# Kernel tuning notes

Measured on AMD Instinct MI355X. Metric: run time of the kernel, lower is better.

Reference implementation:

```python
import jax, jax.numpy as jnp
import numpy as np

N, NUM_ST, NUM_LT = 8, 256, 4096
C_ST, C_LT, C_LAT = 512, 512, 128
LN_EPS = 1e-3  # keras LayerNormalization default epsilon


def setup_inputs() -> dict:
    key = jax.random.key(0)
    ks = jax.random.split(key, 12)
    w = lambda k, shape, sc=0.05: jax.random.normal(k, shape, jnp.float32) * sc
    return {
        "st_feat": jax.random.normal(ks[0], (N, NUM_ST, 1, 1, C_ST), jnp.float32),
        "lt_feat": jax.random.normal(ks[1], (N, NUM_LT, 1, 1, C_LT), jnp.float32),
        # conv1x1 kernels stored as (in, out) matrices
        "w_st": w(ks[2], (C_ST, C_LAT)),
        "b_st": w(ks[3], (C_LAT,), 0.01),
        "w_lt": w(ks[4], (C_LT, C_LAT)),
        "b_lt": w(ks[5], (C_LAT,), 0.01),
        "w_g": w(ks[6], (C_LT, C_LAT)),
        "b_g": w(ks[7], (C_LAT,), 0.01),
        # LayerNorm over axes [1,2,3,4] of (n, C_LAT, NUM_ST, 1, 1)
        "ln_gamma": 1.0 + w(ks[8], (C_LAT, NUM_ST, 1, 1), 0.02),
        "ln_beta": w(ks[9], (C_LAT, NUM_ST, 1, 1), 0.02),
        # out_conv: Conv3D on tensor with last dim 1 -> in_channels=1, kernel (out,)
        "w_out": w(ks[10], (C_ST,)),
        "b_out": w(ks[11], (C_ST,), 0.01),
    }


def reference(st_feat, lt_feat, w_st, b_st, w_lt, b_lt, w_g, b_g,
              ln_gamma, ln_beta, w_out, b_out):
    n = st_feat.shape[0]
    # 1x1x1 conv projections == matmul over last (channel) dim
    theta = jnp.einsum('nshwc,cd->nshwd', st_feat, w_st) + b_st  # (n,S,1,1,c)
    phi = jnp.einsum('nlhwc,cd->nlhwd', lt_feat, w_lt) + b_lt    # (n,L,1,1,c)
    g = jnp.einsum('nlhwc,cd->nlhwd', lt_feat, w_g) + b_g        # (n,L,1,1,c)
    # Faithful raw reshapes (row-major reinterpretation, as in the TF code)
    theta = theta.reshape(n, C_LAT, NUM_ST)
    phi = phi.reshape(n, C_LAT, NUM_LT)
    g = g.reshape(n, C_LAT, NUM_LT)
    # theta^T @ phi  -> (n, S, L)
    attn = jnp.einsum('ncs,ncl->nsl', theta, phi)
    attn = attn / jnp.sqrt(jnp.asarray(C_LAT, jnp.float32))  # use_scale
    p = jax.nn.softmax(attn, axis=-1)
    # g @ p^T -> (n, c, S)
    out = jnp.einsum('ncl,nsl->ncs', g, p)
    out = out.reshape(n, C_LAT, NUM_ST, 1, 1)
    # pre_activate: LayerNorm over all non-batch axes, then ReLU
    mean = jnp.mean(out, axis=(1, 2, 3, 4), keepdims=True)
    var = jnp.var(out, axis=(1, 2, 3, 4), keepdims=True)
    out = (out - mean) * jax.lax.rsqrt(var + LN_EPS) * ln_gamma + ln_beta
    out = jax.nn.relu(out)
    # out_conv: last dim is 1 -> broadcasts to C_ST output channels
    out = out * w_out + b_out  # (n, C_LAT, NUM_ST, 1, C_ST)
    # dropout is identity at inference
    return out
```

## Files before the change

kernel.cpp:

```cpp
#include <hip/hip_runtime.h>
#include <cstdint>

typedef unsigned short u16;
typedef unsigned int u32;
typedef __attribute__((ext_vector_type(8))) __bf16 bf16x8;
typedef __attribute__((ext_vector_type(4))) float f32x4;

__device__ __forceinline__ u32 f2bf_bits(float x) {
    u32 a = __builtin_bit_cast(u32, x);
    a += 0x7FFFu + ((a >> 16) & 1u);
    return a >> 16;
}
__device__ __forceinline__ u32 pack2(float lo, float hi) {
    u32 a = __builtin_bit_cast(u32, lo);
    u32 b = __builtin_bit_cast(u32, hi);
    a += 0x7FFFu + ((a >> 16) & 1u);
    b += 0x7FFFu + ((b >> 16) & 1u);
    return (a >> 16) | (b & 0xFFFF0000u);
}

#define LDS_STRIDE 72

__global__ __launch_bounds__(256) void k_prep(
    const float* __restrict__ w_lt, const float* __restrict__ w_g,
    u16* __restrict__ wltT, u16* __restrict__ wgT,
    const float* __restrict__ st, const float* __restrict__ w_st,
    const float* __restrict__ b_st, u16* __restrict__ thT,
    float* __restrict__ stats)
{
    __shared__ float sA[8 * 512];
    int bi = blockIdx.x;
    int tid = threadIdx.x;
    if (bi < 512) {
        int idx = bi * 256 + tid;
        int which = idx >> 16;
        int rem = idx & 65535;
        int nrow = rem >> 9;
        int k = rem & 511;
        const float* src = which ? w_g : w_lt;
        u16* dst = which ? wgT : wltT;
        dst[rem] = (u16)f2bf_bits(src[k * 128 + nrow]);
        return;
    }
    if (bi == 768) {
        if (tid < 16) stats[tid] = 0.f;
        return;
    }
    int r0 = (bi - 512) * 8;
    {
        const float4* src = (const float4*)(st + (size_t)r0 * 512);
        float4* dst = (float4*)sA;
        #pragma unroll
        for (int i = 0; i < 4; i++) dst[tid + i * 256] = src[tid + i * 256];
    }
    __syncthreads();
    int d = tid & 127, rh = tid >> 7;
    float acc[4] = {0.f, 0.f, 0.f, 0.f};
    #pragma unroll 4
    for (int k = 0; k < 512; k++) {
        float w = w_st[(size_t)k * 128 + d];
        #pragma unroll
        for (int j = 0; j < 4; j++) acc[j] += sA[(rh + j * 2) * 512 + k] * w;
    }
    float bias = b_st[d];
    #pragma unroll
    for (int j = 0; j < 4; j++) {
        int r = r0 + rh + j * 2;
        int n_idx = r >> 8, s_raw = r & 255;
        int f = s_raw * 128 + d;
        thT[(size_t)n_idx * 32768 + (size_t)(f & 255) * 128 + (f >> 8)] =
            (u16)f2bf_bits(acc[j] + bias);
    }
}

__global__ __launch_bounds__(256, 2) void k1_proj_lt(
    const float* __restrict__ lt,
    const u16* __restrict__ wltT, const u16* __restrict__ wgT,
    const float* __restrict__ b_lt, const float* __restrict__ b_g,
    u16* __restrict__ phi, u16* __restrict__ g)
{
    __shared__ u16 sA[128 * LDS_STRIDE];
    __shared__ u16 sBl[128 * LDS_STRIDE];
    __shared__ u16 sBg[128 * LDS_STRIDE];
    int tid = threadIdx.x;
    int wave = tid >> 6, lane = tid & 63, quad = lane >> 4, lq = lane & 15;
    int m0 = blockIdx.x * 128;
    int srow = tid >> 1, skc = (tid & 1) * 32;

    f32x4 zero = {0.f, 0.f, 0.f, 0.f};
    f32x4 acc[2][2][8];
    for (int p = 0; p < 2; p++)
        for (int mt = 0; mt < 2; mt++)
            for (int nt = 0; nt < 8; nt++) acc[p][mt][nt] = zero;

    for (int ko = 0; ko < 8; ko++) {
        {
            const float4* src = (const float4*)(lt + (size_t)(m0 + srow) * 512 + ko * 64 + skc);
            uint2* dst = (uint2*)&sA[srow * LDS_STRIDE + skc];
            #pragma unroll
            for (int i = 0; i < 8; i++) {
                float4 v = src[i];
                uint2 u; u.x = pack2(v.x, v.y); u.y = pack2(v.z, v.w);
                dst[i] = u;
            }
        }
        {
            const uint4* srcl = (const uint4*)(wltT + srow * 512 + ko * 64 + skc);
            const uint4* srcg = (const uint4*)(wgT  + srow * 512 + ko * 64 + skc);
            uint4* dstl = (uint4*)&sBl[srow * LDS_STRIDE + skc];
            uint4* dstg = (uint4*)&sBg[srow * LDS_STRIDE + skc];
            #pragma unroll
            for (int i = 0; i < 4; i++) { dstl[i] = srcl[i]; dstg[i] = srcg[i]; }
        }
        __syncthreads();
        #pragma unroll
        for (int kk = 0; kk < 2; kk++) {
            bf16x8 a[2], bl[8], bg[8];
            #pragma unroll
            for (int mt = 0; mt < 2; mt++)
                a[mt] = *(const bf16x8*)&sA[(wave * 32 + mt * 16 + lq) * LDS_STRIDE + kk * 32 + quad * 8];
            #pragma unroll
            for (int nt = 0; nt < 8; nt++) {
                bl[nt] = *(const bf16x8*)&sBl[(nt * 16 + lq) * LDS_STRIDE + kk * 32 + quad * 8];
                bg[nt] = *(const bf16x8*)&sBg[(nt * 16 + lq) * LDS_STRIDE + kk * 32 + quad * 8];
            }
            #pragma unroll
            for (int mt = 0; mt < 2; mt++)
                #pragma unroll
                for (int nt = 0; nt < 8; nt++) {
                    acc[0][mt][nt] = __builtin_amdgcn_mfma_f32_16x16x32_bf16(a[mt], bl[nt], acc[0][mt][nt], 0, 0, 0);
                    acc[1][mt][nt] = __builtin_amdgcn_mfma_f32_16x16x32_bf16(a[mt], bg[nt], acc[1][mt][nt], 0, 0, 0);
                }
        }
        __syncthreads();
    }
    #pragma unroll
    for (int mt = 0; mt < 2; mt++) {
        int mbase = m0 + wave * 32 + mt * 16 + quad * 4;
        #pragma unroll
        for (int nt = 0; nt < 8; nt++) {
            int n = nt * 16 + lq;
            float biasl = b_lt[n], biasg = b_g[n];
            #pragma unroll
            for (int r = 0; r < 4; r++) {
                size_t o = (size_t)(mbase + r) * 128 + n;
                phi[o] = (u16)f2bf_bits(acc[0][mt][nt][r] + biasl);
                g[o]   = (u16)f2bf_bits(acc[1][mt][nt][r] + biasg);
            }
        }
    }
}

__global__ __launch_bounds__(256) void k_tr(const u16* __restrict__ phi, u16* __restrict__ phiT)
{
    __shared__ u16 s[64 * 65];
    int bi = blockIdx.x;
    int n_idx = bi >> 7, rem = bi & 127;
    int c0 = (rem >> 6) * 64, l0 = (rem & 63) * 64;
    const u16* src = phi + (size_t)n_idx * 524288;
    u16* dst = phiT + (size_t)n_idx * 524288;
    int t = threadIdx.x;
    #pragma unroll
    for (int i = 0; i < 2; i++) {
        int idx = t + i * 256;
        int row = idx >> 3;
        int col = (idx & 7) * 8;
        uint4 v = *(const uint4*)(src + (size_t)(c0 + row) * 4096 + l0 + col);
        u16 tmp[8];
        *(uint4*)tmp = v;
        #pragma unroll
        for (int j = 0; j < 8; j++) s[row * 65 + col + j] = tmp[j];
    }
    __syncthreads();
    #pragma unroll
    for (int i = 0; i < 2; i++) {
        int idx = t + i * 256;
        int lrow = idx >> 3;
        int cb = (idx & 7) * 8;
        u16 tmp[8];
        #pragma unroll
        for (int j = 0; j < 8; j++) tmp[j] = s[(cb + j) * 65 + lrow];
        *(uint4*)(dst + (size_t)(l0 + lrow) * 128 + c0 + cb) = *(uint4*)tmp;
    }
}

__global__ __launch_bounds__(256, 2) void k3_attn(
    const u16* __restrict__ thT, const u16* __restrict__ phiT,
    float* __restrict__ attn)
{
    __shared__ u16 sA[128 * LDS_STRIDE];
    __shared__ u16 sB[128 * LDS_STRIDE];
    int tid = threadIdx.x;
    int wave = tid >> 6, lane = tid & 63, quad = lane >> 4, lq = lane & 15;
    int bi = blockIdx.x;
    int n_idx = bi >> 6, rem = bi & 63;
    int m0 = (rem >> 5) * 128;
    int l0 = (rem & 31) * 128;
    const u16* Ab = thT + (size_t)n_idx * 32768;
    const u16* Bb = phiT + (size_t)n_idx * 524288;
    int srow = tid >> 1, skc = (tid & 1) * 32;

    f32x4 zero = {0.f, 0.f, 0.f, 0.f};
    f32x4 acc[2][8];
    for (int mt = 0; mt < 2; mt++)
        for (int nt = 0; nt < 8; nt++) acc[mt][nt] = zero;

    for (int ko = 0; ko < 2; ko++) {
        const uint4* srcA = (const uint4*)(Ab + (size_t)(m0 + srow) * 128 + ko * 64 + skc);
        const uint4* srcB = (const uint4*)(Bb + (size_t)(l0 + srow) * 128 + ko * 64 + skc);
        uint4* dA = (uint4*)&sA[srow * LDS_STRIDE + skc];
        uint4* dB = (uint4*)&sB[srow * LDS_STRIDE + skc];
        #pragma unroll
        for (int i = 0; i < 4; i++) { dA[i] = srcA[i]; dB[i] = srcB[i]; }
        __syncthreads();
        #pragma unroll
        for (int kk = 0; kk < 2; kk++) {
            bf16x8 a[2], b[8];
            #pragma unroll
            for (int mt = 0; mt < 2; mt++)
                a[mt] = *(const bf16x8*)&sA[(wave * 32 + mt * 16 + lq) * LDS_STRIDE + kk * 32 + quad * 8];
            #pragma unroll
            for (int nt = 0; nt < 8; nt++)
                b[nt] = *(const bf16x8*)&sB[(nt * 16 + lq) * LDS_STRIDE + kk * 32 + quad * 8];
            #pragma unroll
            for (int mt = 0; mt < 2; mt++)
                #pragma unroll
                for (int nt = 0; nt < 8; nt++)
                    acc[mt][nt] = __builtin_amdgcn_mfma_f32_16x16x32_bf16(a[mt], b[nt], acc[mt][nt], 0, 0, 0);
        }
        __syncthreads();
    }
    const float scale = 0.08838834764831845f;
    float* Cb = attn + (size_t)n_idx * 1048576;
    #pragma unroll
    for (int mt = 0; mt < 2; mt++) {
        int mbase = m0 + wave * 32 + mt * 16 + quad * 4;
        #pragma unroll
        for (int nt = 0; nt < 8; nt++) {
            int col = l0 + nt * 16 + lq;
            #pragma unroll
            for (int r = 0; r < 4; r++)
                Cb[(size_t)(mbase + r) * 4096 + col] = acc[mt][nt][r] * scale;
        }
    }
}

__global__ __launch_bounds__(256) void k4_stats(
    const float* __restrict__ attn, float* __restrict__ rowstat)
{
    __shared__ float red[256];
    int r = blockIdx.x;
    int tid = threadIdx.x;
    const float4* src = (const float4*)(attn + (size_t)r * 4096);
    float4 vv[4];
    float m = -1e30f;
    #pragma unroll
    for (int i = 0; i < 4; i++) {
        vv[i] = src[i * 256 + tid];
        m = fmaxf(m, fmaxf(fmaxf(vv[i].x, vv[i].y), fmaxf(vv[i].z, vv[i].w)));
    }
    red[tid] = m;
    __syncthreads();
    for (int s = 128; s > 0; s >>= 1) {
        if (tid < s) red[tid] = fmaxf(red[tid], red[tid + s]);
        __syncthreads();
    }
    m = red[0];
    __syncthreads();
    float sum = 0.f;
    #pragma unroll
    for (int i = 0; i < 4; i++) {
        vv[i].x = __expf(vv[i].x - m); vv[i].y = __expf(vv[i].y - m);
        vv[i].z = __expf(vv[i].z - m); vv[i].w = __expf(vv[i].w - m);
        sum += vv[i].x + vv[i].y + vv[i].z + vv[i].w;
    }
    red[tid] = sum;
    __syncthreads();
    for (int s = 128; s > 0; s >>= 1) {
        if (tid < s) red[tid] += red[tid + s];
        __syncthreads();
    }
    if (tid == 0) {
        rowstat[r * 2]     = m;
        rowstat[r * 2 + 1] = 1.0f / red[0];
    }
}

__global__ __launch_bounds__(256, 2) void k5_pv(
    const u16* __restrict__ g, const float* __restrict__ attn,
    const float* __restrict__ rowstat,
    float* __restrict__ opart)
{
    __shared__ u16 sA[128 * LDS_STRIDE];
    __shared__ u16 sB[128 * LDS_STRIDE];
    int tid = threadIdx.x;
    int wave = tid >> 6, lane = tid & 63, quad = lane >> 4, lq = lane & 15;
    int bi = blockIdx.x;
    int n_idx = bi >> 5, rem = bi & 31;
    int kch = rem >> 1, stile = rem & 1;
    int s0 = stile * 128;
    int l_base = kch * 256;
    const u16* Ab = g + (size_t)n_idx * 524288;
    int srow = tid >> 1, skc = (tid & 1) * 32;

    int sr_row = n_idx * 256 + s0 + srow;
    float rm   = rowstat[sr_row * 2];
    float rinv = rowstat[sr_row * 2 + 1];
    const float* Brow = attn + (size_t)sr_row * 4096;

    f32x4 zero = {0.f, 0.f, 0.f, 0.f};
    f32x4 acc[2][8];
    for (int mt = 0; mt < 2; mt++)
        for (int nt = 0; nt < 8; nt++) acc[mt][nt] = zero;

    for (int ko = 0; ko < 4; ko++) {
        int l0 = l_base + ko * 64;
        const uint4* srcA = (const uint4*)(Ab + (size_t)srow * 4096 + l0 + skc);
        const float4* srcB = (const float4*)(Brow + l0 + skc);
        uint4* dA = (uint4*)&sA[srow * LDS_STRIDE + skc];
        uint2* dB = (uint2*)&sB[srow * LDS_STRIDE + skc];
        #pragma unroll
        for (int i = 0; i < 4; i++) dA[i] = srcA[i];
        #pragma unroll
        for (int i = 0; i < 8; i++) {
            float4 v = srcB[i];
            uint2 u;
            u.x = pack2(__expf(v.x - rm) * rinv, __expf(v.y - rm) * rinv);
            u.y = pack2(__expf(v.z - rm) * rinv, __expf(v.w - rm) * rinv);
            dB[i] = u;
        }
        __syncthreads();
        #pragma unroll
        for (int kk = 0; kk < 2; kk++) {
            bf16x8 a[2], b[8];
            #pragma unroll
            for (int mt = 0; mt < 2; mt++)
                a[mt] = *(const bf16x8*)&sA[(wave * 32 + mt * 16 + lq) * LDS_STRIDE + kk * 32 + quad * 8];
            #pragma unroll
            for (int nt = 0; nt < 8; nt++)
                b[nt] = *(const bf16x8*)&sB[(nt * 16 + lq) * LDS_STRIDE + kk * 32 + quad * 8];
            #pragma unroll
            for (int mt = 0; mt < 2; mt++)
                #pragma unroll
                for (int nt = 0; nt < 8; nt++)
                    acc[mt][nt] = __builtin_amdgcn_mfma_f32_16x16x32_bf16(a[mt], b[nt], acc[mt][nt], 0, 0, 0);
        }
        __syncthreads();
    }
    float* Cb = opart + (size_t)(kch * 8 + n_idx) * 32768;
    #pragma unroll
    for (int mt = 0; mt < 2; mt++) {
        int cbase = wave * 32 + mt * 16 + quad * 4;
        #pragma unroll
        for (int nt = 0; nt < 8; nt++) {
            int s = s0 + nt * 16 + lq;
            #pragma unroll
            for (int r = 0; r < 4; r++)
                Cb[(size_t)(cbase + r) * 256 + s] = acc[mt][nt][r];
        }
    }
}

__global__ __launch_bounds__(256) void k5b_reduce(
    const float* __restrict__ opart, float* __restrict__ obuf,
    float* __restrict__ stats)
{
    __shared__ float red[256];
    __shared__ float red2[256];
    int tid = threadIdx.x;
    int bi = blockIdx.x;
    int n_idx = bi >> 4, part = bi & 15;
    int base = part * 2048;
    float lsum = 0.f, lsq = 0.f;
    for (int j = 0; j < 8; j++) {
        int idx = base + j * 256 + tid;
        float o = 0.f;
        #pragma unroll
        for (int ch = 0; ch < 16; ch++)
            o += opart[(size_t)(ch * 8 + n_idx) * 32768 + idx];
        obuf[(size_t)n_idx * 32768 + idx] = o;
        lsum += o; lsq += o * o;
    }
    red[tid] = lsum; red2[tid] = lsq;
    __syncthreads();
    for (int s = 128; s > 0; s >>= 1) {
        if (tid < s) { red[tid] += red[tid + s]; red2[tid] += red2[tid + s]; }
        __syncthreads();
    }
    if (tid == 0) {
        atomicAdd(&stats[n_idx * 2], red[0]);
        atomicAdd(&stats[n_idx * 2 + 1], red2[0]);
    }
}

__global__ __launch_bounds__(256) void k7_out(
    const float* __restrict__ obuf, const float* __restrict__ stats,
    const float* __restrict__ gamma, const float* __restrict__ beta,
    const float* __restrict__ w_out, const float* __restrict__ b_out,
    float* __restrict__ out)
{
    int tid = threadIdx.x;
    long long base = (long long)blockIdx.x * 1024;
    int r0 = blockIdx.x * 8 + (tid >> 7);
    int k4i = tid & 127;
    int n_idx = r0 >> 15;
    float sum = stats[n_idx * 2], sq = stats[n_idx * 2 + 1];
    float mean = sum * (1.0f / 32768.0f);
    float var = sq * (1.0f / 32768.0f) - mean * mean;
    float rstd = rsqrtf(var + 1e-3f);
    const f32x4* w4p = (const f32x4*)w_out;
    const f32x4* b4p = (const f32x4*)b_out;
    f32x4 w4 = w4p[k4i];
    f32x4 b4 = b4p[k4i];
    f32x4* out4 = (f32x4*)out;
    #pragma unroll
    for (int i = 0; i < 4; i++) {
        int row = r0 + i * 2;
        int ridx = row & 32767;
        float o = obuf[row];
        float v = (o - mean) * rstd * gamma[ridx] + beta[ridx];
        v = fmaxf(v, 0.f);
        f32x4 r;
        r.x = __builtin_fmaf(v, w4.x, b4.x);
        r.y = __builtin_fmaf(v, w4.y, b4.y);
        r.z = __builtin_fmaf(v, w4.z, b4.z);
        r.w = __builtin_fmaf(v, w4.w, b4.w);
        __builtin_nontemporal_store(r, &out4[base + tid + i * 256]);
    }
}

extern "C" void kernel_launch(void* const* d_in, const int* in_sizes, int n_in,
                              void* d_out, int out_size, void* d_ws, size_t ws_size,
                              hipStream_t stream)
{
    (void)in_sizes; (void)n_in; (void)out_size; (void)ws_size;
    const float* st    = (const float*)d_in[0];
    const float* lt    = (const float*)d_in[1];
    const float* w_st  = (const float*)d_in[2];
    const float* b_st  = (const float*)d_in[3];
    const float* w_lt  = (const float*)d_in[4];
    const float* b_lt  = (const float*)d_in[5];
    const float* w_g   = (const float*)d_in[6];
    const float* b_g   = (const float*)d_in[7];
    const float* gamma = (const float*)d_in[8];
    const float* beta  = (const float*)d_in[9];
    const float* w_out = (const float*)d_in[10];
    const float* b_out = (const float*)d_in[11];

    char* ws = (char*)d_ws;
    u16*   phi    = (u16*)  (ws + 0);
    u16*   gbuf   = (u16*)  (ws + 8388608);
    u16*   thT    = (u16*)  (ws + 16777216);
    u16*   wltT   = (u16*)  (ws + 17301504);
    u16*   wgT    = (u16*)  (ws + 17432576);
    float* attn   = (float*)(ws + 17563648);
    float* rowstat= (float*)(ws + 51118080);
    float* opart  = (float*)(ws + 67895296);
    float* obuf   = (float*)(ws + 84672512);
    float* stats  = (float*)(ws + 85721088);
    u16*   phiT   = (u16*)opart;

    k_prep     <<<769,   256, 0, stream>>>(w_lt, w_g, wltT, wgT, st, w_st, b_st, thT, stats);
    k1_proj_lt <<<256,   256, 0, stream>>>(lt, wltT, wgT, b_lt, b_g, phi, gbuf);
    k_tr       <<<1024,  256, 0, stream>>>(phi, phiT);
    k3_attn    <<<512,   256, 0, stream>>>(thT, phiT, attn);
    k4_stats   <<<2048,  256, 0, stream>>>(attn, rowstat);
    k5_pv      <<<256,   256, 0, stream>>>(gbuf, attn, rowstat, opart);
    k5b_reduce <<<128,   256, 0, stream>>>(opart, obuf, stats);
    k7_out     <<<32768, 256, 0, stream>>>(obuf, stats, gamma, beta, w_out, b_out,
                                           (float*)d_out);
}
```

Before: 702.2 us.

## Move theta projection into lt projection kernel, split PV over more blocks

The st/theta projection moves out of the weight-prep kernel and runs as extra blocks of the lt projection kernel, so both projections run concurrently. The PV kernel's split-K grid is doubled to 512 blocks with half the K per block, and the reduce kernel is reworked to sum 32 partials over 512 blocks. Block reductions in the stats and reduce kernels now use wave shuffles instead of a full shared-memory tree. The extra partials double the opart traffic, and the buffer offsets are relocated so opart fits.

```diff
diff --git a/kernel.cpp b/kernel.cpp
--- a/kernel.cpp
+++ b/kernel.cpp
@@ -21,70 +21,73 @@
 
 #define LDS_STRIDE 72
 
-__global__ __launch_bounds__(256) void k_prep(
+__global__ __launch_bounds__(256) void k_wt(
     const float* __restrict__ w_lt, const float* __restrict__ w_g,
     u16* __restrict__ wltT, u16* __restrict__ wgT,
-    const float* __restrict__ st, const float* __restrict__ w_st,
-    const float* __restrict__ b_st, u16* __restrict__ thT,
     float* __restrict__ stats)
 {
-    __shared__ float sA[8 * 512];
-    int bi = blockIdx.x;
-    int tid = threadIdx.x;
-    if (bi < 512) {
-        int idx = bi * 256 + tid;
-        int which = idx >> 16;
-        int rem = idx & 65535;
-        int nrow = rem >> 9;
-        int k = rem & 511;
-        const float* src = which ? w_g : w_lt;
-        u16* dst = which ? wgT : wltT;
-        dst[rem] = (u16)f2bf_bits(src[k * 128 + nrow]);
-        return;
-    }
-    if (bi == 768) {
+    int bi = blockIdx.x;
+    int tid = threadIdx.x;
+    if (bi == 512) {
         if (tid < 16) stats[tid] = 0.f;
         return;
     }
-    int r0 = (bi - 512) * 8;
-    {
-        const float4* src = (const float4*)(st + (size_t)r0 * 512);
-        float4* dst = (float4*)sA;
-        #pragma unroll
-        for (int i = 0; i < 4; i++) dst[tid + i * 256] = src[tid + i * 256];
-    }
-    __syncthreads();
-    int d = tid & 127, rh = tid >> 7;
-    float acc[4] = {0.f, 0.f, 0.f, 0.f};
-    #pragma unroll 4
-    for (int k = 0; k < 512; k++) {
-        float w = w_st[(size_t)k * 128 + d];
-        #pragma unroll
-        for (int j = 0; j < 4; j++) acc[j] += sA[(rh + j * 2) * 512 + k] * w;
-    }
-    float bias = b_st[d];
-    #pragma unroll
-    for (int j = 0; j < 4; j++) {
-        int r = r0 + rh + j * 2;
-        int n_idx = r >> 8, s_raw = r & 255;
-        int f = s_raw * 128 + d;
-        thT[(size_t)n_idx * 32768 + (size_t)(f & 255) * 128 + (f >> 8)] =
-            (u16)f2bf_bits(acc[j] + bias);
-    }
+    int idx = bi * 256 + tid;
+    int which = idx >> 16;
+    int rem = idx & 65535;
+    int nrow = rem >> 9;
+    int k = rem & 511;
+    const float* src = which ? w_g : w_lt;
+    u16* dst = which ? wgT : wltT;
+    dst[rem] = (u16)f2bf_bits(src[k * 128 + nrow]);
 }
 
 __global__ __launch_bounds__(256, 2) void k1_proj_lt(
     const float* __restrict__ lt,
     const u16* __restrict__ wltT, const u16* __restrict__ wgT,
     const float* __restrict__ b_lt, const float* __restrict__ b_g,
-    u16* __restrict__ phi, u16* __restrict__ g)
-{
-    __shared__ u16 sA[128 * LDS_STRIDE];
+    u16* __restrict__ phi, u16* __restrict__ g,
+    const float* __restrict__ st, const float* __restrict__ w_st,
+    const float* __restrict__ b_st, u16* __restrict__ thT)
+{
+    __shared__ __align__(16) u16 sA[128 * LDS_STRIDE];
     __shared__ u16 sBl[128 * LDS_STRIDE];
     __shared__ u16 sBg[128 * LDS_STRIDE];
     int tid = threadIdx.x;
+    int bi = blockIdx.x;
+
+    if (bi >= 256) {
+        float* sT = (float*)sA;
+        int r0 = (bi - 256) * 8;
+        {
+            const float4* src = (const float4*)(st + (size_t)r0 * 512);
+            float4* dst = (float4*)sT;
+            #pragma unroll
+            for (int i = 0; i < 4; i++) dst[tid + i * 256] = src[tid + i * 256];
+        }
+        __syncthreads();
+        int d = tid & 127, rh = tid >> 7;
+        float acc[4] = {0.f, 0.f, 0.f, 0.f};
+        #pragma unroll 4
+        for (int k = 0; k < 512; k++) {
+            float w = w_st[(size_t)k * 128 + d];
+            #pragma unroll
+            for (int j = 0; j < 4; j++) acc[j] += sT[(rh + j * 2) * 512 + k] * w;
+        }
+        float bias = b_st[d];
+        #pragma unroll
+        for (int j = 0; j < 4; j++) {
+            int r = r0 + rh + j * 2;
+            int n_idx = r >> 8;
+            int f = (r & 255) * 128 + d;
+            thT[(size_t)n_idx * 32768 + (size_t)(f & 255) * 128 + (f >> 8)] =
+                (u16)f2bf_bits(acc[j] + bias);
+        }
+        return;
+    }
+
     int wave = tid >> 6, lane = tid & 63, quad = lane >> 4, lq = lane & 15;
-    int m0 = blockIdx.x * 128;
+    int m0 = bi * 128;
     int srow = tid >> 1, skc = (tid & 1) * 32;
 
     f32x4 zero = {0.f, 0.f, 0.f, 0.f};
@@ -261,10 +264,15 @@
     }
     red[tid] = m;
     __syncthreads();
-    for (int s = 128; s > 0; s >>= 1) {
-        if (tid < s) red[tid] = fmaxf(red[tid], red[tid + s]);
-        __syncthreads();
-    }
+    if (tid < 128) red[tid] = fmaxf(red[tid], red[tid + 128]);
+    __syncthreads();
+    if (tid < 64) {
+        float v = fmaxf(red[tid], red[tid + 64]);
+        #pragma unroll
+        for (int s = 32; s > 0; s >>= 1) v = fmaxf(v, __shfl_down(v, s));
+        if (tid == 0) red[0] = v;
+    }
+    __syncthreads();
     m = red[0];
     __syncthreads();
     float sum = 0.f;
@@ -276,13 +284,16 @@
     }
     red[tid] = sum;
     __syncthreads();
-    for (int s = 128; s > 0; s >>= 1) {
-        if (tid < s) red[tid] += red[tid + s];
-        __syncthreads();
-    }
-    if (tid == 0) {
-        rowstat[r * 2]     = m;
-        rowstat[r * 2 + 1] = 1.0f / red[0];
+    if (tid < 128) red[tid] += red[tid + 128];
+    __syncthreads();
+    if (tid < 64) {
+        float v = red[tid] + red[tid + 64];
+        #pragma unroll
+        for (int s = 32; s > 0; s >>= 1) v += __shfl_down(v, s);
+        if (tid == 0) {
+            rowstat[r * 2]     = m;
+            rowstat[r * 2 + 1] = 1.0f / v;
+        }
     }
 }
 
@@ -296,10 +307,10 @@
     int tid = threadIdx.x;
     int wave = tid >> 6, lane = tid & 63, quad = lane >> 4, lq = lane & 15;
     int bi = blockIdx.x;
-    int n_idx = bi >> 5, rem = bi & 31;
+    int n_idx = bi >> 6, rem = bi & 63;
     int kch = rem >> 1, stile = rem & 1;
     int s0 = stile * 128;
-    int l_base = kch * 256;
+    int l_base = kch * 128;
     const u16* Ab = g + (size_t)n_idx * 524288;
     int srow = tid >> 1, skc = (tid & 1) * 32;
 
@@ -313,7 +324,7 @@
     for (int mt = 0; mt < 2; mt++)
         for (int nt = 0; nt < 8; nt++) acc[mt][nt] = zero;
 
-    for (int ko = 0; ko < 4; ko++) {
+    for (int ko = 0; ko < 2; ko++) {
         int l0 = l_base + ko * 64;
         const uint4* srcA = (const uint4*)(Ab + (size_t)srow * 4096 + l0 + skc);
         const float4* srcB = (const float4*)(Brow + l0 + skc);
@@ -369,27 +380,35 @@
     __shared__ float red2[256];
     int tid = threadIdx.x;
     int bi = blockIdx.x;
-    int n_idx = bi >> 4, part = bi & 15;
-    int base = part * 2048;
+    int n_idx = bi >> 6, part = bi & 63;
+    int base = part * 512;
     float lsum = 0.f, lsq = 0.f;
-    for (int j = 0; j < 8; j++) {
+    #pragma unroll
+    for (int j = 0; j < 2; j++) {
         int idx = base + j * 256 + tid;
         float o = 0.f;
         #pragma unroll
-        for (int ch = 0; ch < 16; ch++)
+        for (int ch = 0; ch < 32; ch++)
             o += opart[(size_t)(ch * 8 + n_idx) * 32768 + idx];
         obuf[(size_t)n_idx * 32768 + idx] = o;
         lsum += o; lsq += o * o;
     }
     red[tid] = lsum; red2[tid] = lsq;
     __syncthreads();
-    for (int s = 128; s > 0; s >>= 1) {
-        if (tid < s) { red[tid] += red[tid + s]; red2[tid] += red2[tid + s]; }
-        __syncthreads();
-    }
-    if (tid == 0) {
-        atomicAdd(&stats[n_idx * 2], red[0]);
-        atomicAdd(&stats[n_idx * 2 + 1], red2[0]);
+    if (tid < 128) { red[tid] += red[tid + 128]; red2[tid] += red2[tid + 128]; }
+    __syncthreads();
+    if (tid < 64) {
+        float v = red[tid] + red[tid + 64];
+        float v2 = red2[tid] + red2[tid + 64];
+        #pragma unroll
+        for (int s = 32; s > 0; s >>= 1) {
+            v  += __shfl_down(v, s);
+            v2 += __shfl_down(v2, s);
+        }
+        if (tid == 0) {
+            atomicAdd(&stats[n_idx * 2], v);
+            atomicAdd(&stats[n_idx * 2 + 1], v2);
+        }
     }
 }
 
@@ -455,18 +474,19 @@
     u16*   wgT    = (u16*)  (ws + 17432576);
     float* attn   = (float*)(ws + 17563648);
     float* rowstat= (float*)(ws + 51118080);
-    float* opart  = (float*)(ws + 67895296);
-    float* obuf   = (float*)(ws + 84672512);
-    float* stats  = (float*)(ws + 85721088);
+    float* opart  = (float*)(ws + 51134464);
+    float* obuf   = (float*)(ws + 84688896);
+    float* stats  = (float*)(ws + 85737472);
     u16*   phiT   = (u16*)opart;
 
-    k_prep     <<<769,   256, 0, stream>>>(w_lt, w_g, wltT, wgT, st, w_st, b_st, thT, stats);
-    k1_proj_lt <<<256,   256, 0, stream>>>(lt, wltT, wgT, b_lt, b_g, phi, gbuf);
+    k_wt       <<<513,   256, 0, stream>>>(w_lt, w_g, wltT, wgT, stats);
+    k1_proj_lt <<<512,   256, 0, stream>>>(lt, wltT, wgT, b_lt, b_g, phi, gbuf,
+                                           st, w_st, b_st, thT);
     k_tr       <<<1024,  256, 0, stream>>>(phi, phiT);
     k3_attn    <<<512,   256, 0, stream>>>(thT, phiT, attn);
     k4_stats   <<<2048,  256, 0, stream>>>(attn, rowstat);
-    k5_pv      <<<256,   256, 0, stream>>>(gbuf, attn, rowstat, opart);
-    k5b_reduce <<<128,   256, 0, stream>>>(opart, obuf, stats);
+    k5_pv      <<<512,   256, 0, stream>>>(gbuf, attn, rowstat, opart);
+    k5b_reduce <<<512,   256, 0, stream>>>(opart, obuf, stats);
     k7_out     <<<32768, 256, 0, stream>>>(obuf, stats, gamma, beta, w_out, b_out,
                                            (float*)d_out);
 }
```

Result: no change. 695.7 us (-0.9%).
